# Kernel optimization log

Hardware: AMD Instinct MI355X
Metric: run time of the kernel (lower is better)

Reference implementation:

```python
import jax, jax.numpy as jnp
import numpy as np

N_BITS = 16
V = 1 << N_BITS  # 65536 possible 16-bit patterns


def setup_inputs() -> dict:
    key = jax.random.key(0)
    k1, k2, k3 = jax.random.split(key, 3)
    B, H, T = 16, 128, 4096
    W = jax.random.normal(k1, (B, H, N_BITS), dtype=jnp.float32) * 0.5  # per-bit weights
    r = jax.random.normal(k2, (B, H), dtype=jnp.float32)                 # per-hidden phase/bias
    # x holds raw 16-bit patterns (indices into the 2^16 support)
    x = jax.random.randint(k3, (B, T), 0, V, dtype=jnp.int32)
    return {"x": x, "W": W, "r": r}


def _logits_all(W, r):
    """Logit of every one of the 2^16 representable values. [B, V]"""
    enum = jnp.arange(V, dtype=jnp.int32)
    shifts = jnp.arange(N_BITS, dtype=jnp.int32)
    bits = ((enum[:, None] >> shifts[None, :]) & 1).astype(W.dtype)  # [V, N]
    z = jnp.einsum('vn,bhn->bvh', bits, W) + r[:, None, :]           # [B, V, H]
    return jnp.cos(z).sum(axis=-1)                                    # [B, V]


def reference(x, W, r):
    """BIDE forward: log_prob(x) = logit(bits(x)) - logsumexp over all 2^N patterns."""
    logits = _logits_all(W, r)                       # [B, V]
    logZ = jax.nn.logsumexp(logits, axis=1)          # [B]  exact partition over full support
    logit_x = jnp.take_along_axis(logits, x, axis=1) # [B, T] gather by bit-pattern index
    return logit_x - logZ[:, None]
```

## Files before the change

kernel.cpp:

```cpp
#include <hip/hip_runtime.h>
#include <hip/hip_bf16.h>

#define BDIM 16
#define HDIM 128
#define TDIM 4096
#define VSZ  65536

typedef __attribute__((ext_vector_type(8))) short bf16x8;
typedef __attribute__((ext_vector_type(4))) float f32x4;

static __device__ __forceinline__ unsigned int f2bf(float f) {
  unsigned int u = __float_as_uint(f);
  return (u + 0x7fffu + ((u >> 16) & 1u)) >> 16;
}

__global__ __launch_bounds__(512) void bide_main(
    const float* __restrict__ W, const float* __restrict__ r,
    const int* __restrict__ x, float* __restrict__ out,
    float* __restrict__ partM, float* __restrict__ partS) {
  __shared__ unsigned int stg[2][64 * 32];
  __shared__ float ldsT[64 * 64];
  __shared__ float red[16];

  int bid = blockIdx.x;
  int b    = bid >> 4;
  int tile = bid & 15;
  int tlo = (tile & 3) * 64;
  int thi = (tile >> 2) * 64;
  int tid = threadIdx.x;

  int tab  = tid >> 8;
  int srow = tid & 63;
  int grp  = (tid >> 6) & 3;
  int sval = (tab ? tlo : thi) + srow;
  int woff = tab ? 0 : 8;
  int swz  = (srow & 7) << 2;

  int l = tid & 63;
  int w = tid >> 6;
  int rowblk = w & 3, colhalf = w >> 2;
  int r15 = l & 15, kl = l >> 4;
  int arow  = rowblk * 16 + r15;
  int brow0 = colhalf * 32 + r15;
  int brow1 = brow0 + 16;

  const float* Wb = W + b * HDIM * 16;
  const float* rb = r + b * HDIM;

  float fb[8];
#pragma unroll
  for (int n = 0; n < 8; ++n) fb[n] = (float)((sval >> n) & 1);

  f32x4 acc0 = {0.f, 0.f, 0.f, 0.f};
  f32x4 acc1 = {0.f, 0.f, 0.f, 0.f};

  const bf16x8* U8 = (const bf16x8*)stg[0];
  const bf16x8* V8 = (const bf16x8*)stg[1];
  unsigned int* stow = stg[tab];

  for (int kc = 0; kc < 4; ++kc) {
    int hbase = kc * 32;
    __syncthreads();
#pragma unroll
    for (int e = 0; e < 8; e += 2) {
      int hp = grp * 8 + e;
      unsigned int uu0, uu1;
#pragma unroll
      for (int p = 0; p < 2; ++p) {
        int h = hbase + hp + p;
        const float* Wp = Wb + h * 16 + woff;
        float sacc = tab ? rb[h] : 0.f;
#pragma unroll
        for (int n = 0; n < 8; ++n) sacc = fmaf(fb[n], Wp[n], sacc);
        float sn, cs;
        __sincosf(sacc, &sn, &cs);
        if (!tab) sn = -sn;
        unsigned int uv = f2bf(cs) | (f2bf(sn) << 16);
        if (p == 0) uu0 = uv; else uu1 = uv;
      }
      int idx = srow * 32 + (hp ^ swz);
      *(uint2*)&stow[idx] = make_uint2(uu0, uu1);
    }
    __syncthreads();

#pragma unroll
    for (int ks = 0; ks < 2; ++ks) {
      bf16x8 a  = U8[arow  * 8 + ((ks * 4 + kl) ^ (arow  & 7))];
      bf16x8 b0 = V8[brow0 * 8 + ((ks * 4 + kl) ^ (brow0 & 7))];
      bf16x8 b1 = V8[brow1 * 8 + ((ks * 4 + kl) ^ (brow1 & 7))];
      acc0 = __builtin_amdgcn_mfma_f32_16x16x32_bf16(a, b0, acc0, 0, 0, 0);
      acc1 = __builtin_amdgcn_mfma_f32_16x16x32_bf16(a, b1, acc1, 0, 0, 0);
    }
  }

  {
    int c0  = colhalf * 32 + r15;
    int rb0 = rowblk * 16 + 4 * kl;
    int sw  = (c0 & 7) << 3;
    *(f32x4*)&ldsT[c0 * 64 + (rb0 ^ sw)]        = acc0;
    *(f32x4*)&ldsT[(c0 + 16) * 64 + (rb0 ^ sw)] = acc1;
  }

  float m = fmaxf(fmaxf(fmaxf(acc0[0], acc0[1]), fmaxf(acc0[2], acc0[3])),
                  fmaxf(fmaxf(acc1[0], acc1[1]), fmaxf(acc1[2], acc1[3])));
#pragma unroll
  for (int off = 1; off < 64; off <<= 1) m = fmaxf(m, __shfl_xor(m, off, 64));
  if (l == 0) red[w] = m;
  __syncthreads();
  float M = red[0];
#pragma unroll
  for (int i = 1; i < 8; ++i) M = fmaxf(M, red[i]);
  float s = 0.f;
#pragma unroll
  for (int q = 0; q < 4; ++q)
    s += __expf(acc0[q] - M) + __expf(acc1[q] - M);
#pragma unroll
  for (int off = 1; off < 64; off <<= 1) s += __shfl_xor(s, off, 64);
  if (l == 0) red[8 + w] = s;
  __syncthreads();
  if (tid == 0) {
    float S = 0.f;
#pragma unroll
    for (int i = 0; i < 8; ++i) S += red[8 + i];
    partM[bid] = M;
    partS[bid] = S;
  }

  const int4* x4 = (const int4*)(x + b * TDIM);
  float* ob = out + b * TDIM;
#pragma unroll
  for (int it = 0; it < 2; ++it) {
    int4 xv = x4[tid + it * 512];
    int tbase = 4 * (tid + it * 512);
    int vv[4] = {xv.x, xv.y, xv.z, xv.w};
#pragma unroll
    for (int j = 0; j < 4; ++j) {
      int v = vv[j];
      int tl = ((v >> 14) << 2) | ((v >> 6) & 3);
      if (tl == tile) {
        int row = (v >> 8) & 63, col = v & 63;
        ob[tbase + j] = ldsT[col * 64 + (row ^ ((col & 7) << 3))];
      }
    }
  }
}

__global__ __launch_bounds__(256) void bide_sub(
    float* __restrict__ out, const float* __restrict__ partM,
    const float* __restrict__ partS) {
  int bid = blockIdx.x;
  int b = bid >> 2, seg = bid & 3;
  float M = -1e30f;
#pragma unroll
  for (int i = 0; i < 16; ++i) M = fmaxf(M, partM[b * 16 + i]);
  float S = 0.f;
#pragma unroll
  for (int i = 0; i < 16; ++i)
    S += partS[b * 16 + i] * __expf(partM[b * 16 + i] - M);
  float logZ = M + __logf(S);
  float4* o4 = (float4*)(out + b * TDIM + seg * 1024);
  float4 v = o4[threadIdx.x];
  v.x -= logZ; v.y -= logZ; v.z -= logZ; v.w -= logZ;
  o4[threadIdx.x] = v;
}

extern "C" void kernel_launch(void* const* d_in, const int* in_sizes, int n_in,
                              void* d_out, int out_size, void* d_ws, size_t ws_size,
                              hipStream_t stream) {
  const int*   x = (const int*)d_in[0];
  const float* W = (const float*)d_in[1];
  const float* r = (const float*)d_in[2];
  float* out = (float*)d_out;

  float* partM = (float*)d_ws;
  float* partS = partM + 256;

  bide_main<<<BDIM * 16, 512, 0, stream>>>(W, r, x, out, partM, partS);
  bide_sub<<<64, 256, 0, stream>>>(out, partM, partS);
}
```

Before: 69.16 us.

## Fuse logZ subtraction into main kernel via last-block atomic counter

Removes the second kernel launch. The last block to finish for each batch row, detected with an atomic counter and threadfences, combines the partial max/sum values and subtracts logZ from the whole output row. It also stages all four K-chunks of the sincos table in LDS at once, so there is one barrier instead of two per chunk, and it prefetches x at kernel start. In exchange it adds a memset launch, larger LDS use that may lower occupancy, and a serialized tail in the last block of each row.

```diff
diff --git a/kernel.cpp b/kernel.cpp
--- a/kernel.cpp
+++ b/kernel.cpp
@@ -4,7 +4,6 @@
 #define BDIM 16
 #define HDIM 128
 #define TDIM 4096
-#define VSZ  65536
 
 typedef __attribute__((ext_vector_type(8))) short bf16x8;
 typedef __attribute__((ext_vector_type(4))) float f32x4;
@@ -17,10 +16,12 @@
 __global__ __launch_bounds__(512) void bide_main(
     const float* __restrict__ W, const float* __restrict__ r,
     const int* __restrict__ x, float* __restrict__ out,
-    float* __restrict__ partM, float* __restrict__ partS) {
-  __shared__ unsigned int stg[2][64 * 32];
+    float* __restrict__ partM, float* __restrict__ partS,
+    int* __restrict__ counter) {
+  __shared__ unsigned int stg[2][64 * 128];
   __shared__ float ldsT[64 * 64];
   __shared__ float red[16];
+  __shared__ int s_last;
 
   int bid = blockIdx.x;
   int b    = bid >> 4;
@@ -47,27 +48,24 @@
   const float* Wb = W + b * HDIM * 16;
   const float* rb = r + b * HDIM;
 
+  const int4* x4 = (const int4*)(x + b * TDIM);
+  int4 xv0 = x4[tid];
+  int4 xv1 = x4[tid + 512];
+
   float fb[8];
 #pragma unroll
   for (int n = 0; n < 8; ++n) fb[n] = (float)((sval >> n) & 1);
 
-  f32x4 acc0 = {0.f, 0.f, 0.f, 0.f};
-  f32x4 acc1 = {0.f, 0.f, 0.f, 0.f};
-
-  const bf16x8* U8 = (const bf16x8*)stg[0];
-  const bf16x8* V8 = (const bf16x8*)stg[1];
   unsigned int* stow = stg[tab];
-
+#pragma unroll
   for (int kc = 0; kc < 4; ++kc) {
-    int hbase = kc * 32;
-    __syncthreads();
 #pragma unroll
     for (int e = 0; e < 8; e += 2) {
       int hp = grp * 8 + e;
       unsigned int uu0, uu1;
 #pragma unroll
       for (int p = 0; p < 2; ++p) {
-        int h = hbase + hp + p;
+        int h = kc * 32 + hp + p;
         const float* Wp = Wb + h * 16 + woff;
         float sacc = tab ? rb[h] : 0.f;
 #pragma unroll
@@ -78,19 +76,25 @@
         unsigned int uv = f2bf(cs) | (f2bf(sn) << 16);
         if (p == 0) uu0 = uv; else uu1 = uv;
       }
-      int idx = srow * 32 + (hp ^ swz);
+      int idx = srow * 128 + kc * 32 + (hp ^ swz);
       *(uint2*)&stow[idx] = make_uint2(uu0, uu1);
     }
-    __syncthreads();
+  }
+  __syncthreads();
 
+  f32x4 acc0 = {0.f, 0.f, 0.f, 0.f};
+  f32x4 acc1 = {0.f, 0.f, 0.f, 0.f};
+  const bf16x8* U8 = (const bf16x8*)stg[0];
+  const bf16x8* V8 = (const bf16x8*)stg[1];
 #pragma unroll
-    for (int ks = 0; ks < 2; ++ks) {
-      bf16x8 a  = U8[arow  * 8 + ((ks * 4 + kl) ^ (arow  & 7))];
-      bf16x8 b0 = V8[brow0 * 8 + ((ks * 4 + kl) ^ (brow0 & 7))];
-      bf16x8 b1 = V8[brow1 * 8 + ((ks * 4 + kl) ^ (brow1 & 7))];
-      acc0 = __builtin_amdgcn_mfma_f32_16x16x32_bf16(a, b0, acc0, 0, 0, 0);
-      acc1 = __builtin_amdgcn_mfma_f32_16x16x32_bf16(a, b1, acc1, 0, 0, 0);
-    }
+  for (int g = 0; g < 8; ++g) {
+    int base = (g >> 1) * 8;
+    int sl = (g & 1) * 4 + kl;
+    bf16x8 a  = U8[arow  * 32 + base + (sl ^ (arow  & 7))];
+    bf16x8 b0 = V8[brow0 * 32 + base + (sl ^ (brow0 & 7))];
+    bf16x8 b1 = V8[brow1 * 32 + base + (sl ^ (brow1 & 7))];
+    acc0 = __builtin_amdgcn_mfma_f32_16x16x32_bf16(a, b0, acc0, 0, 0, 0);
+    acc1 = __builtin_amdgcn_mfma_f32_16x16x32_bf16(a, b1, acc1, 0, 0, 0);
   }
 
   {
@@ -126,11 +130,10 @@
     partS[bid] = S;
   }
 
-  const int4* x4 = (const int4*)(x + b * TDIM);
   float* ob = out + b * TDIM;
 #pragma unroll
   for (int it = 0; it < 2; ++it) {
-    int4 xv = x4[tid + it * 512];
+    int4 xv = it ? xv1 : xv0;
     int tbase = 4 * (tid + it * 512);
     int vv[4] = {xv.x, xv.y, xv.z, xv.w};
 #pragma unroll
@@ -143,25 +146,31 @@
       }
     }
   }
-}
 
-__global__ __launch_bounds__(256) void bide_sub(
-    float* __restrict__ out, const float* __restrict__ partM,
-    const float* __restrict__ partS) {
-  int bid = blockIdx.x;
-  int b = bid >> 2, seg = bid & 3;
-  float M = -1e30f;
+  __syncthreads();
+  if (tid == 0) {
+    __threadfence();
+    s_last = (atomicAdd(&counter[b], 1) == 15);
+  }
+  __syncthreads();
+  if (s_last) {
+    __threadfence();
+    float Mz = -1e30f;
 #pragma unroll
-  for (int i = 0; i < 16; ++i) M = fmaxf(M, partM[b * 16 + i]);
-  float S = 0.f;
+    for (int i = 0; i < 16; ++i) Mz = fmaxf(Mz, partM[b * 16 + i]);
+    float Sz = 0.f;
 #pragma unroll
-  for (int i = 0; i < 16; ++i)
-    S += partS[b * 16 + i] * __expf(partM[b * 16 + i] - M);
-  float logZ = M + __logf(S);
-  float4* o4 = (float4*)(out + b * TDIM + seg * 1024);
-  float4 v = o4[threadIdx.x];
-  v.x -= logZ; v.y -= logZ; v.z -= logZ; v.w -= logZ;
-  o4[threadIdx.x] = v;
+    for (int i = 0; i < 16; ++i)
+      Sz += partS[b * 16 + i] * __expf(partM[b * 16 + i] - Mz);
+    float logZ = Mz + __logf(Sz);
+    float4* o4b = (float4*)(out + b * TDIM);
+#pragma unroll
+    for (int it = 0; it < 2; ++it) {
+      float4 v = o4b[tid + it * 512];
+      v.x -= logZ; v.y -= logZ; v.z -= logZ; v.w -= logZ;
+      o4b[tid + it * 512] = v;
+    }
+  }
 }
 
 extern "C" void kernel_launch(void* const* d_in, const int* in_sizes, int n_in,
@@ -172,9 +181,10 @@
   const float* r = (const float*)d_in[2];
   float* out = (float*)d_out;
 
-  float* partM = (float*)d_ws;
-  float* partS = partM + 256;
+  float* partM   = (float*)d_ws;
+  float* partS   = partM + 256;
+  int*   counter = (int*)(partS + 256);
 
-  bide_main<<<BDIM * 16, 512, 0, stream>>>(W, r, x, out, partM, partS);
-  bide_sub<<<64, 256, 0, stream>>>(out, partM, partS);
+  hipMemsetAsync(counter, 0, BDIM * sizeof(int), stream);
+  bide_main<<<BDIM * 16, 512, 0, stream>>>(W, r, x, out, partM, partS, counter);
 }
```

Result: slower. 82.88 us (+19.8%).
